# Performance work log

Measured on AMD Instinct MI355X. Metric: run time of the kernel, lower is better.

## Reference

```python
import jax, jax.numpy as jnp
import numpy as np

N_IMG, C_IN, H, W = 8, 8, 136, 200
N_INST = 512
CHANNELS = 8
STRIDE = 8
MASK_OUT_STRIDE = 4
# sizes_of_interest + [last*2], per __init__
SOI = jnp.asarray([64.0, 128.0, 256.0, 512.0, 1024.0, 2048.0], dtype=jnp.float32)
W_NUMS = [(C_IN + 2) * CHANNELS, CHANNELS * CHANNELS, CHANNELS]
B_NUMS = [CHANNELS, CHANNELS, 1]
N_PARAMS = sum(W_NUMS) + sum(B_NUMS)  # 169


def compute_locations(h, w, stride):
    # matches adet compute_locations: centers of stride-sized cells, (x, y)
    shifts_x = jnp.arange(w, dtype=jnp.float32) * stride + stride // 2
    shifts_y = jnp.arange(h, dtype=jnp.float32) * stride + stride // 2
    ys, xs = jnp.meshgrid(shifts_y, shifts_x, indexing='ij')
    return jnp.stack([xs.reshape(-1), ys.reshape(-1)], axis=1)  # [h*w, 2]


def bilinear_up_align_corners(x, out_h, out_w):
    # x: [n, h, w]; F.interpolate(mode='bilinear', align_corners=True)
    n, h, w = x.shape
    ys = jnp.linspace(0.0, h - 1.0, out_h)
    xs = jnp.linspace(0.0, w - 1.0, out_w)
    y0 = jnp.floor(ys).astype(jnp.int32)
    x0 = jnp.floor(xs).astype(jnp.int32)
    y1 = jnp.minimum(y0 + 1, h - 1)
    x1 = jnp.minimum(x0 + 1, w - 1)
    wy = (ys - y0.astype(jnp.float32))[None, :, None]
    wx = (xs - x0.astype(jnp.float32))[None, None, :]
    top = x[:, y0, :]
    bot = x[:, y1, :]
    row0 = top[:, :, x0] * (1.0 - wx) + top[:, :, x1] * wx
    row1 = bot[:, :, x0] * (1.0 - wx) + bot[:, :, x1] * wx
    return row0 * (1.0 - wy) + row1 * wy


def dice_coefficient(x, target):
    eps = 1e-5
    n = x.shape[0]
    x = x.reshape(n, -1)
    target = target.reshape(n, -1)
    intersection = jnp.sum(x * target, axis=1)
    union = jnp.sum(x * x, axis=1) + jnp.sum(target * target, axis=1) + eps
    return 1.0 - 2.0 * intersection / union


def setup_inputs() -> dict:
    key = jax.random.key(0)
    ks = jax.random.split(key, 6)
    mask_feats = jax.random.normal(ks[0], (N_IMG, C_IN, H, W), jnp.float32)
    mask_head_params = jax.random.normal(ks[1], (N_INST, N_PARAMS), jnp.float32) * 0.1
    instance_locations = jax.random.uniform(ks[2], (N_INST, 2), jnp.float32) * jnp.asarray(
        [W * STRIDE, H * STRIDE], dtype=jnp.float32)
    gt_masks = (jax.random.uniform(ks[3], (N_INST, 2 * H, 2 * W), jnp.float32) > 0.5).astype(jnp.float32)
    im_inds = jax.random.randint(ks[4], (N_INST,), 0, N_IMG, jnp.int32)
    fpn_levels = jax.random.randint(ks[5], (N_INST,), 0, 5, jnp.int32)
    return {
        'mask_feats': mask_feats,
        'mask_head_params': mask_head_params,
        'instance_locations': instance_locations,
        'gt_masks': gt_masks,
        'im_inds': im_inds,
        'fpn_levels': fpn_levels,
        'mask_feat_stride': 8,
    }


def reference(mask_feats, mask_head_params, instance_locations, gt_masks, im_inds, fpn_levels, mask_feat_stride):
    n_inst = mask_head_params.shape[0]
    # relative coordinates: instance center minus every grid location, / size-of-interest
    locations = compute_locations(H, W, mask_feat_stride)          # [H*W, 2]
    rel = instance_locations[:, None, :] - locations[None, :, :]   # [n, H*W, 2]
    rel = jnp.transpose(rel, (0, 2, 1)) / SOI[fpn_levels][:, None, None]
    rel = rel.reshape(n_inst, 2, H, W)
    feats = mask_feats[im_inds]                                    # gather [n, C_IN, H, W]
    x = jnp.concatenate([rel, feats], axis=1)                      # [n, C_IN+2, H, W]

    # parse_dynamic_params: split per-instance params into 1x1 conv weights/biases
    splits = np.cumsum(W_NUMS + B_NUMS)[:-1].tolist()
    p = jnp.split(mask_head_params, splits, axis=1)
    w0 = p[0].reshape(n_inst, CHANNELS, C_IN + 2)
    w1 = p[1].reshape(n_inst, CHANNELS, CHANNELS)
    w2 = p[2].reshape(n_inst, 1, CHANNELS)
    b0, b1, b2 = p[3], p[4], p[5]

    # grouped 1x1 convs (groups = n_inst) == per-instance channel GEMM
    x = jax.nn.relu(jnp.einsum('nchw,noc->nohw', x, w0) + b0[:, :, None, None])
    x = jax.nn.relu(jnp.einsum('nchw,noc->nohw', x, w1) + b1[:, :, None, None])
    logits = jnp.einsum('nchw,noc->nohw', x, w2) + b2[:, :, None, None]  # [n, 1, H, W]

    up = mask_feat_stride // MASK_OUT_STRIDE
    logits_up = bilinear_up_align_corners(logits[:, 0], H * up, W * up)
    scores = jax.nn.sigmoid(logits_up)
    loss = dice_coefficient(scores, gt_masks)                      # [n]
    return loss
```

## Files before the change

### kernel.cpp

```cpp
#include <hip/hip_runtime.h>
#include <math.h>

#define NIMG 8
#define CIN 8
#define Hh 136
#define Ww 200
#define HW (Hh * Ww)
#define OH 272
#define OW 400
#define NINST 512
#define NPAR 169
#define TROWS 34
#define NTILES 8
#define LROWS 19
#define SPX 512
#define PART_BYTES ((size_t)NINST * NTILES * 3 * 4)

#define PINV(x) asm volatile("" : "+v"(x))
#define PINS(x) asm volatile("" : "+s"(x))
#define MEMFENCE asm volatile("" ::: "memory")

__device__ __forceinline__ void mlp_tile_2p2(
    float* __restrict__ slog, float* __restrict__ hbuf,
    const float* __restrict__ fb0, const float* __restrict__ pp,
    int ly0, int lycnt, int tid,
    const float (&A0)[8], const float (&Ax)[8], const float (&Ay)[8])
{
    const int tpx = lycnt * Ww;
    const float* fbase = fb0 + ly0 * Ww;

    for (int p0 = 0; p0 < tpx; p0 += SPX) {
        const int px  = p0 + tid * 2;
        const bool act = px < tpx;

        MEMFENCE;
        float Wf[64];
#pragma unroll
        for (int o = 0; o < 8; o++)
#pragma unroll
            for (int c = 0; c < 8; c++) Wf[o * 8 + c] = pp[o * 10 + 2 + c];
#pragma unroll
        for (int i = 0; i < 64; i++) PINS(Wf[i]);

        if (act) {
            const int yy = px / 200;
            const int x  = px - yy * 200;
            const float yf = (float)(ly0 + yy);
            const float* fb = fbase + px;
            float f[8][2];
#pragma unroll
            for (int c = 0; c < 8; c++) {
                const float2 t = *reinterpret_cast<const float2*>(fb + c * HW);
                f[c][0] = t.x; f[c][1] = t.y;
            }
#pragma unroll
            for (int o = 0; o < 8; o++) {
                const float pre = A0[o] + Ay[o] * yf;
                float hv[2];
#pragma unroll
                for (int p = 0; p < 2; p++) {
                    const float xf = (float)(x + p);
                    float a = pre + Ax[o] * xf;
#pragma unroll
                    for (int c = 0; c < 8; c++) a += Wf[o * 8 + c] * f[c][p];
                    hv[p] = fmaxf(a, 0.0f);
                }
                *reinterpret_cast<float2*>(&hbuf[o * SPX + tid * 2]) =
                    make_float2(hv[0], hv[1]);
            }
        }
        __syncthreads();

        MEMFENCE;
        float w1[64];
#pragma unroll
        for (int k = 0; k < 64; k++) w1[k] = pp[80 + k];
#pragma unroll
        for (int k = 0; k < 64; k++) PINS(w1[k]);
        float w2[8], b1[8], b2;
#pragma unroll
        for (int k = 0; k < 8; k++) { w2[k] = pp[144 + k]; b1[k] = pp[160 + k]; }
        b2 = pp[168];
#pragma unroll
        for (int k = 0; k < 8; k++) { PINV(w2[k]); PINV(b1[k]); }
        PINV(b2);

        if (act) {
            float h[8][2];
#pragma unroll
            for (int c = 0; c < 8; c++) {
                const float2 t = *reinterpret_cast<const float2*>(
                    &hbuf[c * SPX + tid * 2]);
                h[c][0] = t.x; h[c][1] = t.y;
            }
            float o2[2];
#pragma unroll
            for (int p = 0; p < 2; p++) {
                float g[8];
#pragma unroll
                for (int o = 0; o < 8; o++) {
                    float a = b1[o];
#pragma unroll
                    for (int c = 0; c < 8; c++) a += w1[o * 8 + c] * h[c][p];
                    g[o] = fmaxf(a, 0.0f);
                }
                float lg = b2;
#pragma unroll
                for (int c = 0; c < 8; c++) lg += w2[c] * g[c];
                o2[p] = lg;
            }
            *reinterpret_cast<float2*>(&slog[px]) = make_float2(o2[0], o2[1]);
        }
        __syncthreads();
    }
}

__device__ __forceinline__ void dice_tile(
    const float* __restrict__ slog, const float* __restrict__ gtn,
    int oy0, int ly0, int lycnt, int tid,
    float& aI, float& aS, float& aT)
{
    const float sy = 135.0f / 271.0f;
    const float sx = 199.0f / 399.0f;
    for (int g4 = tid; g4 < TROWS * (OW / 4); g4 += 256) {
        const int ry = g4 / 100;
        const int gx = (g4 - ry * 100) * 4;
        const int oy = oy0 + ry;
        const float ysf = (float)oy * sy;
        const int y0 = (int)ysf;
        const float wy = ysf - (float)y0;
        const int y1 = (y0 + 1 > Hh - 1) ? (Hh - 1) : (y0 + 1);
        int r0i = y0 - ly0, r1i = y1 - ly0;
        r0i = r0i < 0 ? 0 : (r0i > lycnt - 1 ? lycnt - 1 : r0i);
        r1i = r1i < 0 ? 0 : (r1i > lycnt - 1 ? lycnt - 1 : r1i);
        const float* s0 = &slog[r0i * Ww];
        const float* s1 = &slog[r1i * Ww];

        const float4 t4 = *reinterpret_cast<const float4*>(gtn + ry * OW + gx);
        const float tv[4] = { t4.x, t4.y, t4.z, t4.w };
#pragma unroll
        for (int p = 0; p < 4; p++) {
            const int ox = gx + p;
            const float xsf = (float)ox * sx;
            const int x0 = (int)xsf;
            const float wx = xsf - (float)x0;
            const int x1 = (x0 + 1 > Ww - 1) ? (Ww - 1) : (x0 + 1);
            const float v00 = s0[x0];
            const float v01 = s0[x1];
            const float v10 = s1[x0];
            const float v11 = s1[x1];
            const float top = v00 + wx * (v01 - v00);
            const float bot = v10 + wx * (v11 - v10);
            const float v   = top + wy * (bot - top);
            const float s   = __fdividef(1.0f, 1.0f + __expf(-v));
            aI += s * tv[p];
            aS += s * s;
            aT += tv[p];
        }
    }
}

#define LOAD_AFFINE                                                             \
    const float ix = iloc[2 * n + 0];                                           \
    const float iy = iloc[2 * n + 1];                                           \
    const int   im = iminds[n];                                                 \
    const float invsoi = 1.0f / (float)(64 << lvls[n]);                         \
    const float* pp = pars + n * NPAR;                                          \
    float A0[8], Ax[8], Ay[8];                                                  \
    _Pragma("unroll")                                                           \
    for (int o = 0; o < 8; o++) {                                               \
        const float wx0 = pp[o * 10 + 0];                                       \
        const float wy0 = pp[o * 10 + 1];                                       \
        Ax[o] = -8.0f * invsoi * wx0;                                           \
        Ay[o] = -8.0f * invsoi * wy0;                                           \
        A0[o] = pp[152 + o] + (wx0 * (ix - 4.0f) + wy0 * (iy - 4.0f)) * invsoi; \
    }                                                                           \
    _Pragma("unroll")                                                           \
    for (int o = 0; o < 8; o++) { PINV(A0[o]); PINV(Ax[o]); PINV(Ay[o]); }

__global__ __launch_bounds__(256, 5) void dmh_tile(
    const float* __restrict__ feats,
    const float* __restrict__ pars,
    const float* __restrict__ iloc,
    const float* __restrict__ gt,
    const int* __restrict__ iminds,
    const int* __restrict__ lvls,
    float* __restrict__ part)
{
    __shared__ float slog[LROWS * Ww];
    __shared__ float hbuf[8 * SPX];
    __shared__ float sred[12];

    const int n    = blockIdx.y;
    const int tile = blockIdx.x;
    const int tid  = threadIdx.x;

    LOAD_AFFINE

    const float sy = 135.0f / 271.0f;
    const int oy0 = tile * TROWS;
    const int ly0 = (int)((float)oy0 * sy);
    int lyL = (int)((float)(oy0 + TROWS - 1) * sy) + 1;
    if (lyL > Hh - 1) lyL = Hh - 1;
    const int lycnt = lyL - ly0 + 1;

    const float* fb0 = feats + (size_t)im * (CIN * HW);
    mlp_tile_2p2(slog, hbuf, fb0, pp, ly0, lycnt, tid, A0, Ax, Ay);

    float aI = 0.0f, aS = 0.0f, aT = 0.0f;
    const float* gtn = gt + (size_t)n * (OH * OW) + (size_t)oy0 * OW;
    dice_tile(slog, gtn, oy0, ly0, lycnt, tid, aI, aS, aT);

#pragma unroll
    for (int off = 32; off > 0; off >>= 1) {
        aI += __shfl_down(aI, off, 64);
        aS += __shfl_down(aS, off, 64);
        aT += __shfl_down(aT, off, 64);
    }
    const int wv = tid >> 6;
    if ((tid & 63) == 0) {
        sred[wv * 3 + 0] = aI;
        sred[wv * 3 + 1] = aS;
        sred[wv * 3 + 2] = aT;
    }
    __syncthreads();
    if (tid == 0) {
        float* pt = part + (size_t)(n * NTILES + tile) * 3;
        pt[0] = sred[0] + sred[3] + sred[6] + sred[9];
        pt[1] = sred[1] + sred[4] + sred[7] + sred[10];
        pt[2] = sred[2] + sred[5] + sred[8] + sred[11];
    }
}

__global__ __launch_bounds__(256) void dmh_fin2(const float* __restrict__ part,
                                                float* __restrict__ out)
{
    const int i = blockIdx.x * 256 + threadIdx.x;
    if (i < NINST) {
        float I = 0.0f, S = 0.0f, T = 0.0f;
#pragma unroll
        for (int t = 0; t < NTILES; t++) {
            const float* pt = part + (size_t)(i * NTILES + t) * 3;
            I += pt[0]; S += pt[1]; T += pt[2];
        }
        out[i] = 1.0f - 2.0f * I / (S + T + 1e-5f);
    }
}

__global__ __launch_bounds__(256, 5) void dmh_one(
    const float* __restrict__ feats,
    const float* __restrict__ pars,
    const float* __restrict__ iloc,
    const float* __restrict__ gt,
    const int* __restrict__ iminds,
    const int* __restrict__ lvls,
    float* __restrict__ out)
{
    __shared__ float slog[LROWS * Ww];
    __shared__ float hbuf[8 * SPX];
    __shared__ float sred[12];

    const int n   = blockIdx.x;
    const int tid = threadIdx.x;

    LOAD_AFFINE

    const float sy = 135.0f / 271.0f;
    const float* fb0 = feats + (size_t)im * (CIN * HW);

    float aI = 0.0f, aS = 0.0f, aT = 0.0f;
    for (int tile = 0; tile < NTILES; tile++) {
        const int oy0 = tile * TROWS;
        const int ly0 = (int)((float)oy0 * sy);
        int lyL = (int)((float)(oy0 + TROWS - 1) * sy) + 1;
        if (lyL > Hh - 1) lyL = Hh - 1;
        const int lycnt = lyL - ly0 + 1;

        mlp_tile_2p2(slog, hbuf, fb0, pp, ly0, lycnt, tid, A0, Ax, Ay);
        const float* gtn = gt + (size_t)n * (OH * OW) + (size_t)oy0 * OW;
        dice_tile(slog, gtn, oy0, ly0, lycnt, tid, aI, aS, aT);
        __syncthreads();
    }

#pragma unroll
    for (int off = 32; off > 0; off >>= 1) {
        aI += __shfl_down(aI, off, 64);
        aS += __shfl_down(aS, off, 64);
        aT += __shfl_down(aT, off, 64);
    }
    const int wv = tid >> 6;
    if ((tid & 63) == 0) {
        sred[wv * 3 + 0] = aI;
        sred[wv * 3 + 1] = aS;
        sred[wv * 3 + 2] = aT;
    }
    __syncthreads();
    if (tid == 0) {
        const float I = sred[0] + sred[3] + sred[6] + sred[9];
        const float S = sred[1] + sred[4] + sred[7] + sred[10];
        const float T = sred[2] + sred[5] + sred[8] + sred[11];
        out[n] = 1.0f - 2.0f * I / (S + T + 1e-5f);
    }
}

extern "C" void kernel_launch(void* const* d_in, const int* in_sizes, int n_in,
                              void* d_out, int out_size, void* d_ws, size_t ws_size,
                              hipStream_t stream) {
    const float* feats  = (const float*)d_in[0];
    const float* pars   = (const float*)d_in[1];
    const float* iloc   = (const float*)d_in[2];
    const float* gt     = (const float*)d_in[3];
    const int*   iminds = (const int*)d_in[4];
    const int*   lvls   = (const int*)d_in[5];

    if (ws_size >= PART_BYTES) {
        float* part = (float*)d_ws;
        dim3 g(NTILES, NINST);
        dmh_tile<<<g, 256, 0, stream>>>(feats, pars, iloc, gt, iminds, lvls, part);
        dmh_fin2<<<(NINST + 255) / 256, 256, 0, stream>>>(part, (float*)d_out);
    } else {
        dmh_one<<<NINST, 256, 0, stream>>>(feats, pars, iloc, gt, iminds, lvls,
                                           (float*)d_out);
    }
}
```

Baseline: 383.0 us.

## Keep first-layer hidden activations in registers instead of LDS staging buffer

The per-pixel MLP now holds layer-0 outputs in registers and feeds them straight into layer 1, removing the shared-memory hbuf round trip and the two block barriers per pixel chunk. Only one barrier after the whole tile remains. The freed LDS and the launch-bounds change from 5 to 6 blocks per SM aim to raise occupancy. In exchange each thread keeps more live VGPRs across both layers, which risks spills under the tighter register budget.

```diff
diff --git a/kernel.cpp b/kernel.cpp
--- a/kernel.cpp
+++ b/kernel.cpp
@@ -13,26 +13,22 @@
 #define TROWS 34
 #define NTILES 8
 #define LROWS 19
-#define SPX 512
 #define PART_BYTES ((size_t)NINST * NTILES * 3 * 4)
 
 #define PINV(x) asm volatile("" : "+v"(x))
 #define PINS(x) asm volatile("" : "+s"(x))
 #define MEMFENCE asm volatile("" ::: "memory")
-
-__device__ __forceinline__ void mlp_tile_2p2(
-    float* __restrict__ slog, float* __restrict__ hbuf,
-    const float* __restrict__ fb0, const float* __restrict__ pp,
-    int ly0, int lycnt, int tid,
+#define SCHEDBAR __builtin_amdgcn_sched_barrier(0)
+
+__device__ __forceinline__ void mlp_tile_reg(
+    float* __restrict__ slog, const float* __restrict__ fb0,
+    const float* __restrict__ pp, int ly0, int lycnt, int tid,
     const float (&A0)[8], const float (&Ax)[8], const float (&Ay)[8])
 {
     const int tpx = lycnt * Ww;
     const float* fbase = fb0 + ly0 * Ww;
 
-    for (int p0 = 0; p0 < tpx; p0 += SPX) {
-        const int px  = p0 + tid * 2;
-        const bool act = px < tpx;
-
+    for (int px = tid * 2; px < tpx; px += 512) {
         MEMFENCE;
         float Wf[64];
 #pragma unroll
@@ -42,34 +38,32 @@
 #pragma unroll
         for (int i = 0; i < 64; i++) PINS(Wf[i]);
 
-        if (act) {
-            const int yy = px / 200;
-            const int x  = px - yy * 200;
-            const float yf = (float)(ly0 + yy);
-            const float* fb = fbase + px;
-            float f[8][2];
-#pragma unroll
-            for (int c = 0; c < 8; c++) {
-                const float2 t = *reinterpret_cast<const float2*>(fb + c * HW);
-                f[c][0] = t.x; f[c][1] = t.y;
+        const int yy = px / 200;
+        const int x  = px - yy * 200;
+        const float yf = (float)(ly0 + yy);
+        const float* fb = fbase + px;
+        float f[8][2];
+#pragma unroll
+        for (int c = 0; c < 8; c++) {
+            const float2 t = *reinterpret_cast<const float2*>(fb + c * HW);
+            f[c][0] = t.x; f[c][1] = t.y;
+        }
+        float h[8][2];
+#pragma unroll
+        for (int o = 0; o < 8; o++) {
+            const float pre = A0[o] + Ay[o] * yf;
+#pragma unroll
+            for (int p = 0; p < 2; p++) {
+                const float xf = (float)(x + p);
+                float a = pre + Ax[o] * xf;
+#pragma unroll
+                for (int c = 0; c < 8; c++) a += Wf[o * 8 + c] * f[c][p];
+                h[o][p] = fmaxf(a, 0.0f);
             }
-#pragma unroll
-            for (int o = 0; o < 8; o++) {
-                const float pre = A0[o] + Ay[o] * yf;
-                float hv[2];
-#pragma unroll
-                for (int p = 0; p < 2; p++) {
-                    const float xf = (float)(x + p);
-                    float a = pre + Ax[o] * xf;
-#pragma unroll
-                    for (int c = 0; c < 8; c++) a += Wf[o * 8 + c] * f[c][p];
-                    hv[p] = fmaxf(a, 0.0f);
-                }
-                *reinterpret_cast<float2*>(&hbuf[o * SPX + tid * 2]) =
-                    make_float2(hv[0], hv[1]);
-            }
-        }
-        __syncthreads();
+        }
+#pragma unroll
+        for (int o = 0; o < 8; o++) { PINV(h[o][0]); PINV(h[o][1]); }
+        SCHEDBAR;
 
         MEMFENCE;
         float w1[64];
@@ -85,33 +79,24 @@
         for (int k = 0; k < 8; k++) { PINV(w2[k]); PINV(b1[k]); }
         PINV(b2);
 
-        if (act) {
-            float h[8][2];
-#pragma unroll
-            for (int c = 0; c < 8; c++) {
-                const float2 t = *reinterpret_cast<const float2*>(
-                    &hbuf[c * SPX + tid * 2]);
-                h[c][0] = t.x; h[c][1] = t.y;
+        float o2[2];
+#pragma unroll
+        for (int p = 0; p < 2; p++) {
+            float g[8];
+#pragma unroll
+            for (int o = 0; o < 8; o++) {
+                float a = b1[o];
+#pragma unroll
+                for (int c = 0; c < 8; c++) a += w1[o * 8 + c] * h[c][p];
+                g[o] = fmaxf(a, 0.0f);
             }
-            float o2[2];
-#pragma unroll
-            for (int p = 0; p < 2; p++) {
-                float g[8];
-#pragma unroll
-                for (int o = 0; o < 8; o++) {
-                    float a = b1[o];
-#pragma unroll
-                    for (int c = 0; c < 8; c++) a += w1[o * 8 + c] * h[c][p];
-                    g[o] = fmaxf(a, 0.0f);
-                }
-                float lg = b2;
-#pragma unroll
-                for (int c = 0; c < 8; c++) lg += w2[c] * g[c];
-                o2[p] = lg;
-            }
-            *reinterpret_cast<float2*>(&slog[px]) = make_float2(o2[0], o2[1]);
-        }
-        __syncthreads();
+            float lg = b2;
+#pragma unroll
+            for (int c = 0; c < 8; c++) lg += w2[c] * g[c];
+            o2[p] = lg;
+        }
+        *reinterpret_cast<float2*>(&slog[px]) = make_float2(o2[0], o2[1]);
+        SCHEDBAR;
     }
 }
 
@@ -178,7 +163,7 @@
     _Pragma("unroll")                                                           \
     for (int o = 0; o < 8; o++) { PINV(A0[o]); PINV(Ax[o]); PINV(Ay[o]); }
 
-__global__ __launch_bounds__(256, 5) void dmh_tile(
+__global__ __launch_bounds__(256, 6) void dmh_tile(
     const float* __restrict__ feats,
     const float* __restrict__ pars,
     const float* __restrict__ iloc,
@@ -188,7 +173,6 @@
     float* __restrict__ part)
 {
     __shared__ float slog[LROWS * Ww];
-    __shared__ float hbuf[8 * SPX];
     __shared__ float sred[12];
 
     const int n    = blockIdx.y;
@@ -205,7 +189,8 @@
     const int lycnt = lyL - ly0 + 1;
 
     const float* fb0 = feats + (size_t)im * (CIN * HW);
-    mlp_tile_2p2(slog, hbuf, fb0, pp, ly0, lycnt, tid, A0, Ax, Ay);
+    mlp_tile_reg(slog, fb0, pp, ly0, lycnt, tid, A0, Ax, Ay);
+    __syncthreads();
 
     float aI = 0.0f, aS = 0.0f, aT = 0.0f;
     const float* gtn = gt + (size_t)n * (OH * OW) + (size_t)oy0 * OW;
@@ -247,7 +232,7 @@
     }
 }
 
-__global__ __launch_bounds__(256, 5) void dmh_one(
+__global__ __launch_bounds__(256, 6) void dmh_one(
     const float* __restrict__ feats,
     const float* __restrict__ pars,
     const float* __restrict__ iloc,
@@ -257,7 +242,6 @@
     float* __restrict__ out)
 {
     __shared__ float slog[LROWS * Ww];
-    __shared__ float hbuf[8 * SPX];
     __shared__ float sred[12];
 
     const int n   = blockIdx.x;
@@ -276,7 +260,8 @@
         if (lyL > Hh - 1) lyL = Hh - 1;
         const int lycnt = lyL - ly0 + 1;
 
-        mlp_tile_2p2(slog, hbuf, fb0, pp, ly0, lycnt, tid, A0, Ax, Ay);
+        mlp_tile_reg(slog, fb0, pp, ly0, lycnt, tid, A0, Ax, Ay);
+        __syncthreads();
         const float* gtn = gt + (size_t)n * (OH * OW) + (size_t)oy0 * OW;
         dice_tile(slog, gtn, oy0, ly0, lycnt, tid, aI, aS, aT);
         __syncthreads();
```

Measured after the change: 394.6 us. 3.0% more time.
